# Performance work log

Hardware: AMD Instinct MI355X
Metric: run time of the kernel (lower is better)

## Reference

```python
import jax, jax.numpy as jnp
import numpy as np

EMBED_DIM = 256
BATCH = 2
SEQ = 1024


def setup_inputs() -> dict:
    key = jax.random.key(0)
    ks = jax.random.split(key, 9)
    d = EMBED_DIM
    s = 1.0 / np.sqrt(d)
    return {
        "x": jax.random.normal(ks[0], (BATCH, SEQ, d), dtype=jnp.float32),
        "Wq": jax.random.uniform(ks[1], (d, d), jnp.float32, -s, s),
        "bq": jax.random.uniform(ks[2], (d,), jnp.float32, -s, s),
        "Wk": jax.random.uniform(ks[3], (d, d), jnp.float32, -s, s),
        "bk": jax.random.uniform(ks[4], (d,), jnp.float32, -s, s),
        "Wv": jax.random.uniform(ks[5], (d, d), jnp.float32, -s, s),
        "bv": jax.random.uniform(ks[6], (d,), jnp.float32, -s, s),
        "Wo": jax.random.uniform(ks[7], (d, d), jnp.float32, -s, s),
        "bo": jax.random.uniform(ks[8], (d,), jnp.float32, -s, s),
    }


def reference(x, Wq, bq, Wk, bk, Wv, bv, Wo, bo):
    d = x.shape[-1]
    Q = x @ Wq.T + bq  # (B,S,D)
    K = x @ Wk.T + bk
    V = x @ Wv.T + bv
    # geodesic_distance with metric='exponential': L2 norm of pairwise diffs
    diff = Q[:, :, None, :] - K[:, None, :, :]          # (B,S,S,D)
    dist = jnp.sqrt(jnp.sum(diff * diff, axis=-1))      # (B,S,S)
    attn = jax.nn.softmax(-dist / jnp.sqrt(jnp.float32(d)), axis=-1)
    attended = jnp.einsum('bqk,bkd->bqd', attn, V)      # (B,S,D)
    return attended @ Wo.T + bo
```

## Files before the change

kernel.cpp:

```cpp
#include <hip/hip_runtime.h>
#include <hip/hip_bf16.h>

#define BB 2
#define SS 1024
#define DD 256
#define NCH 4
#define KCH 256

typedef __attribute__((ext_vector_type(8))) short bf16x8;
typedef __attribute__((ext_vector_type(4))) float f32x4;

__device__ __forceinline__ unsigned short f2bf(float f) {
    __hip_bfloat16 h = __float2bfloat16(f);
    return *reinterpret_cast<unsigned short*>(&h);
}
__device__ __forceinline__ float bf2f(unsigned short u) {
    __hip_bfloat16 h;
    *reinterpret_cast<unsigned short*>(&h) = u;
    return __bfloat162float(h);
}
__device__ __forceinline__ bf16x8 cvt8(float4 f0, float4 f1) {
    bf16x8 o;
    o[0] = (short)f2bf(f0.x); o[1] = (short)f2bf(f0.y);
    o[2] = (short)f2bf(f0.z); o[3] = (short)f2bf(f0.w);
    o[4] = (short)f2bf(f1.x); o[5] = (short)f2bf(f1.y);
    o[6] = (short)f2bf(f1.z); o[7] = (short)f2bf(f1.w);
    return o;
}

__global__ __launch_bounds__(256) void cvt_w(
    const float* __restrict__ Wq, const float* __restrict__ Wk,
    const float* __restrict__ Wv, const float* __restrict__ Wo,
    unsigned short* __restrict__ Wqb, unsigned short* __restrict__ Wkb,
    unsigned short* __restrict__ Wvb, unsigned short* __restrict__ Wob)
{
    const int u = blockIdx.x * 256 + threadIdx.x;
    const float* src;
    unsigned short* dst;
    int base;
    if (u < 8192)       { src = Wq; dst = Wqb; base = u; }
    else if (u < 16384) { src = Wk; dst = Wkb; base = u - 8192; }
    else if (u < 24576) { src = Wv; dst = Wvb; base = u - 16384; }
    else                { src = Wo; dst = Wob; base = u - 24576; }
    const float4* s4 = (const float4*)src + (size_t)base * 2;
    *(bf16x8*)(dst + (size_t)base * 8) = cvt8(s4[0], s4[1]);
}

__global__ __launch_bounds__(256, 2) void qkv_mfma(
    const float* __restrict__ x,
    const unsigned short* __restrict__ Wqb, const float* __restrict__ bq,
    const unsigned short* __restrict__ Wkb, const float* __restrict__ bk,
    const unsigned short* __restrict__ Wvb, const float* __restrict__ bv,
    unsigned short* __restrict__ Qb, unsigned short* __restrict__ Kb,
    unsigned short* __restrict__ VB,
    float* __restrict__ qq, float* __restrict__ kk)
{
    __shared__ float red[4][16];
    const int t = threadIdx.x;
    const int w = t >> 6, l = t & 63, lr = l & 15, lc = l >> 4;
    const int bx = blockIdx.x;
    const int mat = bx % 3;
    const int rest = bx / 3;
    const int tile = rest >> 1;
    const int ch = rest & 1;
    const int r0 = tile * 16;
    const int b = r0 >> 10;
    const int s_in_base = r0 & (SS - 1);
    const size_t rows = (size_t)BB * SS;

    const unsigned short* W = (mat == 0) ? Wqb : (mat == 1) ? Wkb : Wvb;
    const float* bias       = (mat == 0) ? bq  : (mat == 1) ? bk  : bv;

    bf16x8 af[8];
#pragma unroll
    for (int db = 0; db < 8; ++db) {
        const float* xp = x + (size_t)(r0 + lr) * DD + db * 32 + 8 * lc;
        af[db] = cvt8(*(const float4*)(xp), *(const float4*)(xp + 4));
    }

    float nrm[4] = {0.f, 0.f, 0.f, 0.f};

#pragma unroll
    for (int cb = 0; cb < 2; ++cb) {
        const int jb = 128 * ch + 32 * w + 16 * cb;
        f32x4 acc = {0.f, 0.f, 0.f, 0.f};
#pragma unroll
        for (int db = 0; db < 8; ++db) {
            bf16x8 bf = *(const bf16x8*)(W + (size_t)(jb + lr) * DD + db * 32 + 8 * lc);
            acc = __builtin_amdgcn_mfma_f32_16x16x32_bf16(af[db], bf, acc, 0, 0, 0);
        }
        const float bv_ = bias[jb + lr];
#pragma unroll
        for (int r = 0; r < 4; ++r) {
            const int srow = r0 + lc * 4 + r;
            const float v = acc[r] + bv_;
            const unsigned short h = f2bf(v);
            if (mat == 0) {
                Qb[(size_t)srow * DD + jb + lr] = h;
                const float hv = bf2f(h); nrm[r] += hv * hv;
            } else if (mat == 1) {
                Kb[(size_t)srow * DD + jb + lr] = h;
                const float hv = bf2f(h); nrm[r] += hv * hv;
            } else {
                const int s_in = s_in_base + lc * 4 + r;
                const int kb32 = s_in >> 5;
                const int kslot = (s_in >> 3) & 3;
                const int jj = s_in & 7;
                const int db16 = ch * 8 + 2 * w + cb;
                const size_t off = ((size_t)((b * 32 + kb32) * 16 + db16) << 9)
                                 + ((kslot * 16 + lr) << 3) + jj;
                VB[off] = h;
            }
        }
    }

    if (mat < 2) {
#pragma unroll
        for (int r = 0; r < 4; ++r) {
            float n = nrm[r];
#pragma unroll
            for (int m = 1; m < 16; m <<= 1) n += __shfl_xor(n, m, 64);
            if (lr == 0) red[w][lc * 4 + r] = n;
        }
        __syncthreads();
        if (t < 16) {
            const float s = red[0][t] + red[1][t] + red[2][t] + red[3][t];
            if (mat == 0) qq[(size_t)ch * rows + r0 + t] = s;
            else          kk[(size_t)ch * rows + r0 + t] = s;
        }
    }
}

__global__ __launch_bounds__(256, 2) void attn_part_mfma(
    const unsigned short* __restrict__ Qb, const unsigned short* __restrict__ Kb,
    const unsigned short* __restrict__ VB,
    const float* __restrict__ qq, const float* __restrict__ kk,
    float* __restrict__ Opart, float* __restrict__ esum)
{
    __shared__ unsigned short P_s[16 * 256];
    __shared__ float kk_s[KCH];
    __shared__ float qq_s[16];
    __shared__ float es_red[4][16];

    const int t = threadIdx.x;
    const int w = t >> 6, l = t & 63, lr = l & 15, lc = l >> 4;
    const int qtile = blockIdx.x >> 2;
    const int c = blockIdx.x & 3;
    const int rowbase = qtile * 16;
    const int b = rowbase >> 10;
    const int s0 = c * KCH;
    const size_t rows = (size_t)BB * SS;

    kk_s[t] = kk[b * SS + s0 + t] + kk[rows + b * SS + s0 + t];
    if (t < 16) qq_s[t] = qq[rowbase + t] + qq[rows + rowbase + t];

    bf16x8 qf[8];
#pragma unroll
    for (int db = 0; db < 8; ++db)
        qf[db] = *(const bf16x8*)(Qb + (size_t)(rowbase + lr) * DD + db * 32 + 8 * lc);

    __syncthreads();

    float psum[4] = {0.f, 0.f, 0.f, 0.f};
#pragma unroll
    for (int kbi = 0; kbi < 4; ++kbi) {
        const int kb = 64 * w + 16 * kbi;
        f32x4 acc = {0.f, 0.f, 0.f, 0.f};
#pragma unroll
        for (int db = 0; db < 8; ++db) {
            bf16x8 kf = *(const bf16x8*)(
                Kb + (size_t)(b * SS + s0 + kb + lr) * DD + db * 32 + 8 * lc);
            acc = __builtin_amdgcn_mfma_f32_16x16x32_bf16(qf[db], kf, acc, 0, 0, 0);
        }
        const int kcol = kb + lr;
        const float kkv = kk_s[kcol];
#pragma unroll
        for (int r = 0; r < 4; ++r) {
            const int qi = lc * 4 + r;
            const float d2 = fmaxf(qq_s[qi] + kkv - 2.f * acc[r], 0.f);
            const float e = __expf(-sqrtf(d2) * 0.0625f);
            psum[r] += e;
            P_s[qi * 256 + (kcol ^ ((qi & 7) << 3))] = f2bf(e);
        }
    }
#pragma unroll
    for (int r = 0; r < 4; ++r) {
        float s = psum[r];
#pragma unroll
        for (int m = 1; m < 16; m <<= 1) s += __shfl_xor(s, m, 64);
        if (lr == 0) es_red[w][lc * 4 + r] = s;
    }
    __syncthreads();
    if (t < 16)
        esum[(size_t)c * rows + rowbase + t] =
            es_red[0][t] + es_red[1][t] + es_red[2][t] + es_red[3][t];

    f32x4 acc2[4];
#pragma unroll
    for (int i = 0; i < 4; ++i) acc2[i] = (f32x4){0.f, 0.f, 0.f, 0.f};

#pragma unroll
    for (int ki = 0; ki < 8; ++ki) {
        bf16x8 pf = *(const bf16x8*)(
            P_s + lr * 256 + ((32 * ki + 8 * lc) ^ ((lr & 7) << 3)));
        const size_t tbase =
            ((size_t)((b * 32 + c * 8 + ki) * 16 + 4 * w) << 9) + l * 8;
#pragma unroll
        for (int dbi = 0; dbi < 4; ++dbi) {
            bf16x8 vf = *(const bf16x8*)(VB + tbase + ((size_t)dbi << 9));
            acc2[dbi] = __builtin_amdgcn_mfma_f32_16x16x32_bf16(pf, vf, acc2[dbi], 0, 0, 0);
        }
    }
#pragma unroll
    for (int dbi = 0; dbi < 4; ++dbi)
#pragma unroll
        for (int r = 0; r < 4; ++r)
            Opart[((size_t)c * rows + rowbase + lc * 4 + r) * DD
                  + 64 * w + 16 * dbi + lr] = acc2[dbi][r];
}

__global__ __launch_bounds__(256) void reduce_att(
    const float* __restrict__ Opart, const float* __restrict__ esum,
    unsigned short* __restrict__ attb)
{
    const size_t rows = (size_t)BB * SS;
    const int u = blockIdx.x * 256 + threadIdx.x;
    const int row = u >> 5;
    const int d8 = (u & 31) * 8;

    const float inv = 1.f / (esum[row] + esum[rows + row] +
                             esum[2 * rows + row] + esum[3 * rows + row]);

    float s0 = 0.f, s1 = 0.f, s2 = 0.f, s3 = 0.f;
    float s4 = 0.f, s5 = 0.f, s6 = 0.f, s7 = 0.f;
#pragma unroll
    for (int c = 0; c < NCH; ++c) {
        const float* p = Opart + ((size_t)c * rows + row) * DD + d8;
        float4 a0 = *(const float4*)(p);
        float4 a1 = *(const float4*)(p + 4);
        s0 += a0.x; s1 += a0.y; s2 += a0.z; s3 += a0.w;
        s4 += a1.x; s5 += a1.y; s6 += a1.z; s7 += a1.w;
    }
    bf16x8 a;
    a[0] = (short)f2bf(s0 * inv); a[1] = (short)f2bf(s1 * inv);
    a[2] = (short)f2bf(s2 * inv); a[3] = (short)f2bf(s3 * inv);
    a[4] = (short)f2bf(s4 * inv); a[5] = (short)f2bf(s5 * inv);
    a[6] = (short)f2bf(s6 * inv); a[7] = (short)f2bf(s7 * inv);
    *(bf16x8*)(attb + (size_t)row * DD + d8) = a;
}

__global__ __launch_bounds__(256, 2) void outproj_mfma(
    const unsigned short* __restrict__ attb,
    const unsigned short* __restrict__ Wob, const float* __restrict__ bo,
    float* __restrict__ out)
{
    __shared__ unsigned short att_s[16 * 264];
    const int t = threadIdx.x;
    const int w = t >> 6, l = t & 63, lr = l & 15, lc = l >> 4;
    const int r0 = (blockIdx.x >> 2) * 16;
    const int ch = blockIdx.x & 3;

#pragma unroll
    for (int i = 0; i < 2; ++i) {
        const int u = t + i * 256;
        const int row = u >> 5;
        const int d8 = (u & 31) * 8;
        *(bf16x8*)(att_s + row * 264 + d8) =
            *(const bf16x8*)(attb + (size_t)(r0 + row) * DD + d8);
    }
    __syncthreads();

    bf16x8 af[8];
#pragma unroll
    for (int db = 0; db < 8; ++db)
        af[db] = *(const bf16x8*)(att_s + lr * 264 + db * 32 + 8 * lc);

    const int jb = 64 * ch + 16 * w;
    f32x4 acc = {0.f, 0.f, 0.f, 0.f};
#pragma unroll
    for (int db = 0; db < 8; ++db) {
        bf16x8 bf = *(const bf16x8*)(Wob + (size_t)(jb + lr) * DD + db * 32 + 8 * lc);
        acc = __builtin_amdgcn_mfma_f32_16x16x32_bf16(af[db], bf, acc, 0, 0, 0);
    }
    const float bov = bo[jb + lr];
#pragma unroll
    for (int r = 0; r < 4; ++r)
        out[(size_t)(r0 + lc * 4 + r) * DD + jb + lr] = acc[r] + bov;
}

extern "C" void kernel_launch(void* const* d_in, const int* in_sizes, int n_in,
                              void* d_out, int out_size, void* d_ws, size_t ws_size,
                              hipStream_t stream) {
    const float* x  = (const float*)d_in[0];
    const float* Wq = (const float*)d_in[1];
    const float* bq = (const float*)d_in[2];
    const float* Wk = (const float*)d_in[3];
    const float* bk = (const float*)d_in[4];
    const float* Wv = (const float*)d_in[5];
    const float* bv = (const float*)d_in[6];
    const float* Wo = (const float*)d_in[7];
    const float* bo = (const float*)d_in[8];
    float* out = (float*)d_out;

    const size_t rows = (size_t)BB * SS;
    unsigned short* Qb   = (unsigned short*)d_ws;
    unsigned short* Kb   = Qb + rows * DD;
    unsigned short* VB   = Kb + rows * DD;
    unsigned short* Wqb  = VB + rows * DD;
    unsigned short* Wkb  = Wqb + (size_t)DD * DD;
    unsigned short* Wvb  = Wkb + (size_t)DD * DD;
    unsigned short* Wob  = Wvb + (size_t)DD * DD;
    unsigned short* attb = Wob + (size_t)DD * DD;
    float* qq    = (float*)(attb + rows * DD);
    float* kk    = qq + 2 * rows;
    float* esum  = kk + 2 * rows;
    float* Opart = esum + (size_t)NCH * rows;

    cvt_w<<<128, 256, 0, stream>>>(Wq, Wk, Wv, Wo, Wqb, Wkb, Wvb, Wob);
    qkv_mfma<<<768, 256, 0, stream>>>(
        x, Wqb, bq, Wkb, bk, Wvb, bv, Qb, Kb, VB, qq, kk);
    attn_part_mfma<<<(int)(rows / 16) * NCH, 256, 0, stream>>>(
        Qb, Kb, VB, qq, kk, Opart, esum);
    reduce_att<<<256, 256, 0, stream>>>(Opart, esum, attb);
    outproj_mfma<<<(int)(rows / 16) * 4, 256, 0, stream>>>(
        attb, Wob, bo, out);
}
```

Baseline: 48.55 us.

## Process 32 query rows per attention block and split keys into eight chunks

The attention kernel now handles two 16-row query subtiles per block, so each loaded K fragment and V fragment feeds two MFMAs. The key range is split into eight 128-wide chunks instead of four 256-wide ones, which keeps the grid size at 512 blocks. This is meant to cut global K/V traffic per unit of work. In exchange it doubles the partial-output buffer and the reduction traffic in reduce_att, and raises register pressure from the doubled Q fragments and accumulators.

```diff
diff --git a/kernel.cpp b/kernel.cpp
--- a/kernel.cpp
+++ b/kernel.cpp
@@ -4,8 +4,9 @@
 #define BB 2
 #define SS 1024
 #define DD 256
-#define NCH 4
-#define KCH 256
+#define NCH 8
+#define KCH 128
+#define QT 32
 
 typedef __attribute__((ext_vector_type(8))) short bf16x8;
 typedef __attribute__((ext_vector_type(4))) float f32x4;
@@ -137,86 +138,112 @@
     const float* __restrict__ qq, const float* __restrict__ kk,
     float* __restrict__ Opart, float* __restrict__ esum)
 {
-    __shared__ unsigned short P_s[16 * 256];
+    __shared__ unsigned short P_s[QT * KCH];
     __shared__ float kk_s[KCH];
-    __shared__ float qq_s[16];
-    __shared__ float es_red[4][16];
+    __shared__ float qq_s[QT];
+    __shared__ float es_red[4][QT];
 
     const int t = threadIdx.x;
     const int w = t >> 6, l = t & 63, lr = l & 15, lc = l >> 4;
-    const int qtile = blockIdx.x >> 2;
-    const int c = blockIdx.x & 3;
-    const int rowbase = qtile * 16;
+    const int qtile = blockIdx.x >> 3;
+    const int c = blockIdx.x & 7;
+    const int rowbase = qtile * QT;
     const int b = rowbase >> 10;
     const int s0 = c * KCH;
     const size_t rows = (size_t)BB * SS;
 
-    kk_s[t] = kk[b * SS + s0 + t] + kk[rows + b * SS + s0 + t];
-    if (t < 16) qq_s[t] = qq[rowbase + t] + qq[rows + rowbase + t];
-
-    bf16x8 qf[8];
-#pragma unroll
-    for (int db = 0; db < 8; ++db)
-        qf[db] = *(const bf16x8*)(Qb + (size_t)(rowbase + lr) * DD + db * 32 + 8 * lc);
+    if (t < KCH) kk_s[t] = kk[b * SS + s0 + t] + kk[rows + b * SS + s0 + t];
+    if (t < QT)  qq_s[t] = qq[rowbase + t] + qq[rows + rowbase + t];
+
+    bf16x8 qf[2][8];
+#pragma unroll
+    for (int qs = 0; qs < 2; ++qs)
+#pragma unroll
+        for (int db = 0; db < 8; ++db)
+            qf[qs][db] = *(const bf16x8*)(
+                Qb + (size_t)(rowbase + 16 * qs + lr) * DD + db * 32 + 8 * lc);
 
     __syncthreads();
 
-    float psum[4] = {0.f, 0.f, 0.f, 0.f};
-#pragma unroll
-    for (int kbi = 0; kbi < 4; ++kbi) {
-        const int kb = 64 * w + 16 * kbi;
-        f32x4 acc = {0.f, 0.f, 0.f, 0.f};
-#pragma unroll
-        for (int db = 0; db < 8; ++db) {
-            bf16x8 kf = *(const bf16x8*)(
+    float psum[2][4];
+#pragma unroll
+    for (int qs = 0; qs < 2; ++qs)
+#pragma unroll
+        for (int r = 0; r < 4; ++r) psum[qs][r] = 0.f;
+
+#pragma unroll
+    for (int kbi = 0; kbi < 2; ++kbi) {
+        const int kb = 32 * w + 16 * kbi;
+        bf16x8 kf[8];
+#pragma unroll
+        for (int db = 0; db < 8; ++db)
+            kf[db] = *(const bf16x8*)(
                 Kb + (size_t)(b * SS + s0 + kb + lr) * DD + db * 32 + 8 * lc);
-            acc = __builtin_amdgcn_mfma_f32_16x16x32_bf16(qf[db], kf, acc, 0, 0, 0);
-        }
+
         const int kcol = kb + lr;
         const float kkv = kk_s[kcol];
 #pragma unroll
+        for (int qs = 0; qs < 2; ++qs) {
+            f32x4 acc = {0.f, 0.f, 0.f, 0.f};
+#pragma unroll
+            for (int db = 0; db < 8; ++db)
+                acc = __builtin_amdgcn_mfma_f32_16x16x32_bf16(qf[qs][db], kf[db], acc, 0, 0, 0);
+#pragma unroll
+            for (int r = 0; r < 4; ++r) {
+                const int qi = 16 * qs + lc * 4 + r;
+                const float d2 = fmaxf(qq_s[qi] + kkv - 2.f * acc[r], 0.f);
+                const float e = __expf(-sqrtf(d2) * 0.0625f);
+                psum[qs][r] += e;
+                P_s[qi * KCH + (kcol ^ ((qi & 7) << 3))] = f2bf(e);
+            }
+        }
+    }
+#pragma unroll
+    for (int qs = 0; qs < 2; ++qs)
+#pragma unroll
         for (int r = 0; r < 4; ++r) {
-            const int qi = lc * 4 + r;
-            const float d2 = fmaxf(qq_s[qi] + kkv - 2.f * acc[r], 0.f);
-            const float e = __expf(-sqrtf(d2) * 0.0625f);
-            psum[r] += e;
-            P_s[qi * 256 + (kcol ^ ((qi & 7) << 3))] = f2bf(e);
-        }
-    }
-#pragma unroll
-    for (int r = 0; r < 4; ++r) {
-        float s = psum[r];
-#pragma unroll
-        for (int m = 1; m < 16; m <<= 1) s += __shfl_xor(s, m, 64);
-        if (lr == 0) es_red[w][lc * 4 + r] = s;
-    }
+            float s = psum[qs][r];
+#pragma unroll
+            for (int m = 1; m < 16; m <<= 1) s += __shfl_xor(s, m, 64);
+            if (lr == 0) es_red[w][16 * qs + lc * 4 + r] = s;
+        }
     __syncthreads();
-    if (t < 16)
+    if (t < QT)
         esum[(size_t)c * rows + rowbase + t] =
             es_red[0][t] + es_red[1][t] + es_red[2][t] + es_red[3][t];
 
-    f32x4 acc2[4];
-#pragma unroll
-    for (int i = 0; i < 4; ++i) acc2[i] = (f32x4){0.f, 0.f, 0.f, 0.f};
-
-#pragma unroll
-    for (int ki = 0; ki < 8; ++ki) {
-        bf16x8 pf = *(const bf16x8*)(
-            P_s + lr * 256 + ((32 * ki + 8 * lc) ^ ((lr & 7) << 3)));
+    f32x4 acc2[2][4];
+#pragma unroll
+    for (int qs = 0; qs < 2; ++qs)
+#pragma unroll
+        for (int i = 0; i < 4; ++i) acc2[qs][i] = (f32x4){0.f, 0.f, 0.f, 0.f};
+
+#pragma unroll
+    for (int ki = 0; ki < KCH / 32; ++ki) {
+        bf16x8 pf[2];
+#pragma unroll
+        for (int qs = 0; qs < 2; ++qs)
+            pf[qs] = *(const bf16x8*)(
+                P_s + (16 * qs + lr) * KCH + ((32 * ki + 8 * lc) ^ ((lr & 7) << 3)));
         const size_t tbase =
-            ((size_t)((b * 32 + c * 8 + ki) * 16 + 4 * w) << 9) + l * 8;
+            ((size_t)((b * 32 + c * (KCH / 32) + ki) * 16 + 4 * w) << 9) + l * 8;
 #pragma unroll
         for (int dbi = 0; dbi < 4; ++dbi) {
             bf16x8 vf = *(const bf16x8*)(VB + tbase + ((size_t)dbi << 9));
-            acc2[dbi] = __builtin_amdgcn_mfma_f32_16x16x32_bf16(pf, vf, acc2[dbi], 0, 0, 0);
-        }
-    }
-#pragma unroll
-    for (int dbi = 0; dbi < 4; ++dbi)
-#pragma unroll
-        for (int r = 0; r < 4; ++r)
-            Opart[((size_t)c * rows + rowbase + lc * 4 + r) * DD
-                  + 64 * w + 16 * dbi + lr] = acc2[dbi][r];
+#pragma unroll
+            for (int qs = 0; qs < 2; ++qs)
+                acc2[qs][dbi] = __builtin_amdgcn_mfma_f32_16x16x32_bf16(
+                    pf[qs], vf, acc2[qs][dbi], 0, 0, 0);
+        }
+    }
+#pragma unroll
+    for (int qs = 0; qs < 2; ++qs)
+#pragma unroll
+        for (int dbi = 0; dbi < 4; ++dbi)
+#pragma unroll
+            for (int r = 0; r < 4; ++r)
+                Opart[((size_t)c * rows + rowbase + 16 * qs + lc * 4 + r) * DD
+                      + 64 * w + 16 * dbi + lr] = acc2[qs][dbi][r];
 }
 
 __global__ __launch_bounds__(256) void reduce_att(
@@ -228,8 +255,10 @@
     const int row = u >> 5;
     const int d8 = (u & 31) * 8;
 
-    const float inv = 1.f / (esum[row] + esum[rows + row] +
-                             esum[2 * rows + row] + esum[3 * rows + row]);
+    float den = 0.f;
+#pragma unroll
+    for (int c = 0; c < NCH; ++c) den += esum[(size_t)c * rows + row];
+    const float inv = 1.f / den;
 
     float s0 = 0.f, s1 = 0.f, s2 = 0.f, s3 = 0.f;
     float s4 = 0.f, s5 = 0.f, s6 = 0.f, s7 = 0.f;
@@ -319,7 +348,7 @@
     cvt_w<<<128, 256, 0, stream>>>(Wq, Wk, Wv, Wo, Wqb, Wkb, Wvb, Wob);
     qkv_mfma<<<768, 256, 0, stream>>>(
         x, Wqb, bq, Wkb, bk, Wvb, bv, Qb, Kb, VB, qq, kk);
-    attn_part_mfma<<<(int)(rows / 16) * NCH, 256, 0, stream>>>(
+    attn_part_mfma<<<(int)(rows / QT) * NCH, 256, 0, stream>>>(
         Qb, Kb, VB, qq, kk, Opart, esum);
     reduce_att<<<256, 256, 0, stream>>>(Opart, esum, attb);
     outproj_mfma<<<(int)(rows / 16) * 4, 256, 0, stream>>>(
```

After: 47.84 us. About the same (-1.5%).
